# Performance work log

Hardware: AMD Instinct MI355X
Metric: run time of the kernel (lower is better)

Reference implementation:

```python
import jax, jax.numpy as jnp
import numpy as np

B, N, K = 8, 2048, 16
C_IN, C_MID, C_OUT = 64, 16, 64
WH = [32, 32]
FH = [256]


def _mlp_params(key, dims, scale_keyed=True):
    ps = []
    for i in range(len(dims) - 1):
        key, k1 = jax.random.split(key)
        w = jax.random.normal(k1, (dims[i], dims[i + 1]), jnp.float32) / np.sqrt(dims[i])
        b = jnp.zeros((dims[i + 1],), jnp.float32)
        ps += [w, b]
    return ps


def setup_inputs() -> dict:
    key = jax.random.key(0)
    k1, k2, k3, k4, k5 = jax.random.split(key, 5)
    groups = jnp.broadcast_to(jnp.arange(N, dtype=jnp.int32) // K, (B, N))
    points = jax.random.normal(k1, (B, N, 3), jnp.float32)
    feats = jax.random.normal(k2, (B, N, C_IN), jnp.float32)
    point_mask = (jax.random.uniform(k3, (B, N)) > 0.1).astype(jnp.float32)
    w1, b1, w2, b2, w3, b3 = _mlp_params(k4, [3] + WH + [C_MID])
    f1, fb1, f2, fb2 = _mlp_params(k5, [C_IN * C_MID] + FH + [C_OUT])
    return {"groups": groups, "points": points, "feats": feats,
            "point_mask": point_mask,
            "w1": w1, "b1": b1, "w2": w2, "b2": b2, "w3": w3, "b3": b3,
            "f1": f1, "fb1": fb1, "f2": f2, "fb2": fb2}


def _neighbor_idxs(groups):
    # matches[b,i,j] = groups[b,i]==groups[b,j]; torch .nonzero yields, per (b,i),
    # the matching j in increasing order -> stable argsort of ~matches, take first K.
    matches = groups[:, :, None] == groups[:, None, :]            # [B,N,N]
    return jnp.argsort((~matches).astype(jnp.int32), axis=-1)[:, :, :K]  # [B,N,K]


def reference(groups, points, feats, point_mask,
              w1, b1, w2, b2, w3, b3, f1, fb1, f2, fb2):
    idxs = _neighbor_idxs(groups)                                  # [B,N,K] int
    gather = jax.vmap(lambda arr, ix: arr[ix])                     # per-batch gather
    nb_pts = gather(points, idxs)                                  # [B,N,K,3]
    nb_feats = gather(feats, idxs)                                 # [B,N,K,C_IN]
    rel = points[:, :, None, :] - nb_pts                           # [B,N,K,3] (xy encoding = identity)

    # weight_conv: pointwise MLP 3 -> 32 -> 32 -> C_MID, then explicit ReLU
    h = jax.nn.relu(rel @ w1 + b1)
    h = jax.nn.relu(h @ w2 + b2)
    m = jax.nn.relu(h @ w3 + b3)                                   # [B,N,K,C_MID]

    tmask = gather(point_mask, idxs)                               # [B,N,K]
    m = m * tmask[..., None]
    nb_feats = nb_feats * tmask[..., None]

    # per-(point) matmul: [C_MID,K] x [K,C_IN] -> flatten C_MID-major
    e = jnp.einsum('bnkm,bnkc->bnmc', m, nb_feats)                 # [B,N,C_MID,C_IN]
    e = e.reshape(B, N, C_MID * C_IN)

    # final_conv: pointwise MLP 1024 -> 256 -> C_OUT
    h2 = jax.nn.relu(e @ f1 + fb1)
    out = h2 @ f2 + fb2                                            # [B,N,C_OUT]
    return out
```

## Files before the change

kernel.cpp:

```cpp
#include <hip/hip_runtime.h>

typedef unsigned short u16;
typedef short bf16x8 __attribute__((ext_vector_type(8)));
typedef float f32x4  __attribute__((ext_vector_type(4)));
typedef u16   u16x4  __attribute__((ext_vector_type(4)));

__device__ __forceinline__ u16 f2bf(float f) {
  union { float f; unsigned int i; } v; v.f = f;
  unsigned int r = (v.i + 0x7FFFu + ((v.i >> 16) & 1u)) >> 16;
  return (u16)r;
}

__global__ __launch_bounds__(256) void repack_k(const float* __restrict__ f1,
                                                const float* __restrict__ f2,
                                                u16* __restrict__ f1p,
                                                u16* __restrict__ f2p) {
  const int o = blockIdx.x * 256 + threadIdx.x;
  if (o < 262144) {
    const int j = o & 7, n = (o >> 3) & 255, kb = o >> 11;
    f1p[o] = f2bf(f1[(kb * 8 + j) * 256 + n]);
  }
  if (o < 16384) {
    const int j = o & 7, n = (o >> 3) & 63, kb = o >> 9;
    f2p[o] = f2bf(f2[(kb * 8 + j) * 64 + n]);
  }
}

__global__ __launch_bounds__(256) void mlp_einsum_k(
    const float* __restrict__ points, const float* __restrict__ feats,
    const float* __restrict__ pmask,
    const float* __restrict__ w1, const float* __restrict__ b1,
    const float* __restrict__ w2, const float* __restrict__ b2,
    const float* __restrict__ w3, const float* __restrict__ b3,
    const float* __restrict__ f1, const float* __restrict__ f2,
    u16* __restrict__ f1p, u16* __restrict__ f2p,
    u16* __restrict__ Eg) {
  const int gi = blockIdx.x;
  const int bb = blockIdx.y;
  const int base = gi * 16;
  const int t = threadIdx.x;

  __shared__ float Wl[1712];
  __shared__ float Pl[16][3];
  __shared__ float Mask[16];
  __shared__ float F[1024];
  __shared__ float Ml[16 * 16 * 17];

  {
    const int o = (bb * 128 + gi) * 256 + t;
    { const int j = o & 7, n = (o >> 3) & 255, kb = o >> 11;
      f1p[o] = f2bf(f1[(kb * 8 + j) * 256 + n]); }
    if (o < 16384) {
      const int j = o & 7, n = (o >> 3) & 63, kb = o >> 9;
      f2p[o] = f2bf(f2[(kb * 8 + j) * 64 + n]);
    }
  }

  for (int idx = t; idx < 96;   idx += 256) Wl[idx]        = w1[idx];
  for (int idx = t; idx < 32;   idx += 256) Wl[96 + idx]   = b1[idx];
  for (int idx = t; idx < 1024; idx += 256) Wl[128 + idx]  = w2[idx];
  for (int idx = t; idx < 32;   idx += 256) Wl[1152 + idx] = b2[idx];
  for (int idx = t; idx < 512;  idx += 256) Wl[1184 + idx] = w3[idx];
  for (int idx = t; idx < 16;   idx += 256) Wl[1696 + idx] = b3[idx];
  if (t < 16) {
    Mask[t] = pmask[bb * 2048 + base + t];
    const int p = (bb * 2048 + base + t) * 3;
    Pl[t][0] = points[p + 0];
    Pl[t][1] = points[p + 1];
    Pl[t][2] = points[p + 2];
  }
  __syncthreads();

  for (int e = t; e < 1024; e += 256) {
    const int k = e >> 6;
    F[e] = feats[(bb * 2048 + base) * 64 + e] * Mask[k];
  }
  {
    const int i = t >> 4, k = t & 15;
    const float r0 = Pl[i][0] - Pl[k][0];
    const float r1 = Pl[i][1] - Pl[k][1];
    const float r2 = Pl[i][2] - Pl[k][2];
    float h1[32];
#pragma unroll
    for (int o = 0; o < 32; ++o) {
      float a = Wl[96 + o];
      a = fmaf(r0, Wl[o], a);
      a = fmaf(r1, Wl[32 + o], a);
      a = fmaf(r2, Wl[64 + o], a);
      h1[o] = fmaxf(a, 0.f);
    }
    float h2[32];
#pragma unroll
    for (int o = 0; o < 32; ++o) h2[o] = Wl[1152 + o];
#pragma unroll
    for (int j = 0; j < 32; ++j) {
      const float hj = h1[j];
      const float* w = &Wl[128 + j * 32];
#pragma unroll
      for (int o = 0; o < 32; ++o) h2[o] = fmaf(hj, w[o], h2[o]);
    }
#pragma unroll
    for (int o = 0; o < 32; ++o) h2[o] = fmaxf(h2[o], 0.f);
    float mo[16];
#pragma unroll
    for (int o = 0; o < 16; ++o) mo[o] = Wl[1696 + o];
#pragma unroll
    for (int j = 0; j < 32; ++j) {
      const float hj = h2[j];
      const float* w = &Wl[1184 + j * 16];
#pragma unroll
      for (int o = 0; o < 16; ++o) mo[o] = fmaf(hj, w[o], mo[o]);
    }
    const float mk = Mask[k];
    float* Mrow = &Ml[(i * 16 + k) * 17];
#pragma unroll
    for (int o = 0; o < 16; ++o) Mrow[o] = fmaxf(mo[o], 0.f) * mk;
  }
  __syncthreads();

  {
    const int i = t >> 4;
    const int c0 = (t & 15) * 4;
    float acc[16][4] = {};
#pragma unroll
    for (int k = 0; k < 16; ++k) {
      const float* Fr = &F[k * 64 + c0];
      const float f0 = Fr[0], fA = Fr[1], fB = Fr[2], fC = Fr[3];
      const float* Mrow = &Ml[(i * 16 + k) * 17];
#pragma unroll
      for (int mi = 0; mi < 16; ++mi) {
        const float mv = Mrow[mi];
        acc[mi][0] = fmaf(mv, f0, acc[mi][0]);
        acc[mi][1] = fmaf(mv, fA, acc[mi][1]);
        acc[mi][2] = fmaf(mv, fB, acc[mi][2]);
        acc[mi][3] = fmaf(mv, fC, acc[mi][3]);
      }
    }
    u16* Erow = Eg + (size_t)(bb * 2048 + base + i) * 1024;
#pragma unroll
    for (int mi = 0; mi < 16; ++mi) {
      u16x4 v = { f2bf(acc[mi][0]), f2bf(acc[mi][1]),
                  f2bf(acc[mi][2]), f2bf(acc[mi][3]) };
      *(u16x4*)&Erow[mi * 64 + c0] = v;
    }
  }
}

#define STAGE(bf_, kc_)                                                        \
  do {                                                                         \
    const int rl_ = lane >> 3;                                       \
    const int sg_ = (lane & 7) ^ rl_;         \
    const u16* s0_ =                                                           \
        Eg + (size_t)(R + wv * 8 + rl_) * 1024 + (kc_) + sg_ * 8;              \
    u16* d0_ = &Asw[bf_][(wv * 8) * 64];            \
    u16* d1_ = &Asw[bf_][(32 + wv * 8) * 64];                                  \
    __builtin_amdgcn_global_load_lds(                                          \
        (const __attribute__((address_space(1))) void*)s0_,                    \
        (__attribute__((address_space(3))) void*)d0_, 16, 0, 0);               \
    __builtin_amdgcn_global_load_lds(                                          \
        (const __attribute__((address_space(1))) void*)(s0_ + 32 * 1024),      \
        (__attribute__((address_space(3))) void*)d1_, 16, 0, 0);               \
  } while (0)

__global__ __launch_bounds__(256) void gemm_k(
    const u16* __restrict__ Eg, const u16* __restrict__ f1p,
    const float* __restrict__ fb1, const u16* __restrict__ f2p,
    const float* __restrict__ fb2, float* __restrict__ out) {
  const int R = blockIdx.x * 64;
  const int t = threadIdx.x;
  const int wv = t >> 6, lane = t & 63;
  const int q = lane >> 4, r16 = lane & 15;

  __shared__ __align__(16) u16 Asw[2][64 * 64];
  __shared__ __align__(16) u16 H2[64 * 264];

  const int nb = wv * 64;
  f32x4 acc[4][4] = {};

  STAGE(0, 0);
  for (int c = 0; c < 16; ++c) {
    const int bf = c & 1;
    asm volatile("s_waitcnt vmcnt(0)" ::: "memory");
    __builtin_amdgcn_s_barrier();

    bf16x8 bv[2][4];
#pragma unroll
    for (int ksl = 0; ksl < 2; ++ksl) {
      const int kb = c * 8 + ksl * 4 + q;
#pragma unroll
      for (int nt = 0; nt < 4; ++nt)
        bv[ksl][nt] =
            *(const bf16x8*)&f1p[(size_t)(kb * 256 + nb + nt * 16 + r16) * 8];
    }
    bf16x8 a[2][4];
#pragma unroll
    for (int ksl = 0; ksl < 2; ++ksl)
#pragma unroll
      for (int rt = 0; rt < 4; ++rt) {
        const int r = rt * 16 + r16;
        const int g = (ksl * 4 + q) ^ (r & 7);
        a[ksl][rt] = *(const bf16x8*)&Asw[bf][r * 64 + g * 8];
      }
    __builtin_amdgcn_sched_barrier(0);
    if (c < 15) STAGE(bf ^ 1, (c + 1) * 64);
    __builtin_amdgcn_sched_barrier(0);
#pragma unroll
    for (int ksl = 0; ksl < 2; ++ksl)
#pragma unroll
      for (int nt = 0; nt < 4; ++nt)
#pragma unroll
        for (int rt = 0; rt < 4; ++rt)
          acc[rt][nt] = __builtin_amdgcn_mfma_f32_16x16x32_bf16(
              a[ksl][rt], bv[ksl][nt], acc[rt][nt], 0, 0, 0);
    __builtin_amdgcn_s_barrier();
  }

#pragma unroll
  for (int nt = 0; nt < 4; ++nt) {
    const int col = nb + nt * 16 + r16;
    const float bias = fb1[col];
#pragma unroll
    for (int rt = 0; rt < 4; ++rt)
#pragma unroll
      for (int r = 0; r < 4; ++r)
        H2[(rt * 16 + q * 4 + r) * 264 + col] =
            f2bf(fmaxf(acc[rt][nt][r] + bias, 0.f));
  }
  __syncthreads();

  const int n0 = wv * 16;
  const float bias2 = fb2[n0 + r16];
#pragma unroll
  for (int rt = 0; rt < 4; ++rt) {
    f32x4 a2 = {};
#pragma unroll
    for (int ks = 0; ks < 8; ++ks) {
      const bf16x8 av = *(const bf16x8*)&H2[(rt * 16 + r16) * 264 + ks * 32 + q * 8];
      const bf16x8 b2v =
          *(const bf16x8*)&f2p[(size_t)((ks * 4 + q) * 64 + n0 + r16) * 8];
      a2 = __builtin_amdgcn_mfma_f32_16x16x32_bf16(av, b2v, a2, 0, 0, 0);
    }
#pragma unroll
    for (int r = 0; r < 4; ++r)
      out[(size_t)(R + rt * 16 + q * 4 + r) * 64 + n0 + r16] = a2[r] + bias2;
  }
}
#undef STAGE

__global__ __launch_bounds__(256) void fused_k(
    const float* __restrict__ points, const float* __restrict__ feats,
    const float* __restrict__ pmask,
    const float* __restrict__ w1, const float* __restrict__ b1,
    const float* __restrict__ w2, const float* __restrict__ b2,
    const float* __restrict__ w3, const float* __restrict__ b3,
    const u16* __restrict__ f1p, const float* __restrict__ fb1,
    const u16* __restrict__ f2p, const float* __restrict__ fb2,
    float* __restrict__ out) {
  const int gi = blockIdx.x;
  const int bb = blockIdx.y;
  const int base = gi * 16;
  const int t = threadIdx.x;

  __shared__ float Wl[1712];
  __shared__ float Pl[16][3];
  __shared__ float Mask[16];
  __shared__ float F[1024];
  __shared__ __align__(16) u16 E[16 * 1032];
  __shared__ __align__(16) union {
    float Ml[16 * 16 * 17];
    u16   H2[16 * 264];
  } U;

  for (int idx = t; idx < 96;   idx += 256) Wl[idx]        = w1[idx];
  for (int idx = t; idx < 32;   idx += 256) Wl[96 + idx]   = b1[idx];
  for (int idx = t; idx < 1024; idx += 256) Wl[128 + idx]  = w2[idx];
  for (int idx = t; idx < 32;   idx += 256) Wl[1152 + idx] = b2[idx];
  for (int idx = t; idx < 512;  idx += 256) Wl[1184 + idx] = w3[idx];
  for (int idx = t; idx < 16;   idx += 256) Wl[1696 + idx] = b3[idx];
  if (t < 16) {
    Mask[t] = pmask[bb * 2048 + base + t];
    const int p = (bb * 2048 + base + t) * 3;
    Pl[t][0] = points[p + 0];
    Pl[t][1] = points[p + 1];
    Pl[t][2] = points[p + 2];
  }
  __syncthreads();

  for (int e = t; e < 1024; e += 256) {
    const int k = e >> 6;
    F[e] = feats[(bb * 2048 + base) * 64 + e] * Mask[k];
  }
  {
    const int i = t >> 4, k = t & 15;
    const float r0 = Pl[i][0] - Pl[k][0];
    const float r1 = Pl[i][1] - Pl[k][1];
    const float r2 = Pl[i][2] - Pl[k][2];
    float h1[32];
#pragma unroll
    for (int o = 0; o < 32; ++o) {
      float a = Wl[96 + o];
      a = fmaf(r0, Wl[o], a);
      a = fmaf(r1, Wl[32 + o], a);
      a = fmaf(r2, Wl[64 + o], a);
      h1[o] = fmaxf(a, 0.f);
    }
    float h2[32];
#pragma unroll
    for (int o = 0; o < 32; ++o) h2[o] = Wl[1152 + o];
#pragma unroll
    for (int j = 0; j < 32; ++j) {
      const float hj = h1[j];
      const float* w = &Wl[128 + j * 32];
#pragma unroll
      for (int o = 0; o < 32; ++o) h2[o] = fmaf(hj, w[o], h2[o]);
    }
#pragma unroll
    for (int o = 0; o < 32; ++o) h2[o] = fmaxf(h2[o], 0.f);
    float mo[16];
#pragma unroll
    for (int o = 0; o < 16; ++o) mo[o] = Wl[1696 + o];
#pragma unroll
    for (int j = 0; j < 32; ++j) {
      const float hj = h2[j];
      const float* w = &Wl[1184 + j * 16];
#pragma unroll
      for (int o = 0; o < 16; ++o) mo[o] = fmaf(hj, w[o], mo[o]);
    }
    const float mk = Mask[k];
    float* Mrow = &U.Ml[(i * 16 + k) * 17];
#pragma unroll
    for (int o = 0; o < 16; ++o) Mrow[o] = fmaxf(mo[o], 0.f) * mk;
  }
  __syncthreads();

  {
    const int i = t >> 4;
    const int c0 = (t & 15) * 4;
    float acc[16][4] = {};
#pragma unroll
    for (int k = 0; k < 16; ++k) {
      const float* Fr = &F[k * 64 + c0];
      const float f0 = Fr[0], fA = Fr[1], fB = Fr[2], fC = Fr[3];
      const float* Mrow = &U.Ml[(i * 16 + k) * 17];
#pragma unroll
      for (int mi = 0; mi < 16; ++mi) {
        const float mv = Mrow[mi];
        acc[mi][0] = fmaf(mv, f0, acc[mi][0]);
        acc[mi][1] = fmaf(mv, fA, acc[mi][1]);
        acc[mi][2] = fmaf(mv, fB, acc[mi][2]);
        acc[mi][3] = fmaf(mv, fC, acc[mi][3]);
      }
    }
    __syncthreads();
#pragma unroll
    for (int mi = 0; mi < 16; ++mi) {
      u16x4 v = { f2bf(acc[mi][0]), f2bf(acc[mi][1]), f2bf(acc[mi][2]), f2bf(acc[mi][3]) };
      *(u16x4*)&E[i * 1032 + mi * 64 + c0] = v;
    }
  }
  __syncthreads();

  {
    const int wv = t >> 6;
    const int lane = t & 63;
    const int q = lane >> 4, r16 = lane & 15;
    const int nb = wv * 64;
    f32x4 acc[4] = {};
    for (int ks = 0; ks < 32; ++ks) {
      const int k0 = ks * 32;
      const bf16x8 a = *(const bf16x8*)&E[r16 * 1032 + k0 + q * 8];
      const int kb = (k0 >> 3) + q;
#pragma unroll
      for (int nt = 0; nt < 4; ++nt) {
        const bf16x8 bvv = *(const bf16x8*)&f1p[(kb * 256 + nb + nt * 16 + r16) * 8];
        acc[nt] = __builtin_amdgcn_mfma_f32_16x16x32_bf16(a, bvv, acc[nt], 0, 0, 0);
      }
    }
    __syncthreads();
#pragma unroll
    for (int nt = 0; nt < 4; ++nt) {
      const int col = nb + nt * 16 + r16;
      const float bias = fb1[col];
#pragma unroll
      for (int r = 0; r < 4; ++r)
        U.H2[(q * 4 + r) * 264 + col] = f2bf(fmaxf(acc[nt][r] + bias, 0.f));
    }
  }
  __syncthreads();

  {
    const int wv = t >> 6;
    const int lane = t & 63;
    const int q = lane >> 4, r16 = lane & 15;
    const int n0 = wv * 16;
    f32x4 acc = {};
#pragma unroll
    for (int ks = 0; ks < 8; ++ks) {
      const int k0 = ks * 32;
      const bf16x8 a = *(const bf16x8*)&U.H2[r16 * 264 + k0 + q * 8];
      const bf16x8 bvv = *(const bf16x8*)&f2p[(((k0 >> 3) + q) * 64 + n0 + r16) * 8];
      acc = __builtin_amdgcn_mfma_f32_16x16x32_bf16(a, bvv, acc, 0, 0, 0);
    }
    const int col = n0 + r16;
    const float bias = fb2[col];
#pragma unroll
    for (int r = 0; r < 4; ++r) {
      const int row = q * 4 + r;
      out[((size_t)(bb * 2048 + base + row)) * 64 + col] = acc[r] + bias;
    }
  }
}

extern "C" void kernel_launch(void* const* d_in, const int* in_sizes, int n_in,
                              void* d_out, int out_size, void* d_ws, size_t ws_size,
                              hipStream_t stream) {
  const float* points = (const float*)d_in[1];
  const float* feats  = (const float*)d_in[2];
  const float* pmask  = (const float*)d_in[3];
  const float* w1 = (const float*)d_in[4];
  const float* b1 = (const float*)d_in[5];
  const float* w2 = (const float*)d_in[6];
  const float* b2 = (const float*)d_in[7];
  const float* w3 = (const float*)d_in[8];
  const float* b3 = (const float*)d_in[9];
  const float* f1 = (const float*)d_in[10];
  const float* fb1 = (const float*)d_in[11];
  const float* f2 = (const float*)d_in[12];
  const float* fb2 = (const float*)d_in[13];
  float* out = (float*)d_out;

  u16* f1p = (u16*)d_ws;
  u16* f2p = f1p + 262144;
  const size_t NEED = 524288 + 32768 + (size_t)16384 * 1024 * 2;

  if (ws_size >= NEED) {
    u16* Eg = f2p + 16384;
    mlp_einsum_k<<<dim3(128, 8), dim3(256), 0, stream>>>(
        points, feats, pmask, w1, b1, w2, b2, w3, b3, f1, f2, f1p, f2p, Eg);
    gemm_k<<<dim3(256), dim3(256), 0, stream>>>(Eg, f1p, fb1, f2p, fb2, out);
  } else {
    repack_k<<<dim3(1024), dim3(256), 0, stream>>>(f1, f2, f1p, f2p);
    fused_k<<<dim3(128, 8), dim3(256), 0, stream>>>(points, feats, pmask,
                                                    w1, b1, w2, b2, w3, b3,
                                                    f1p, fb1, f2p, fb2, out);
  }
}
```

Measured before the change: 140.0 us.

## Triple-buffer GEMM A staging and read MLP weights directly from global

The GEMM kernel moves from a double to a triple LDS buffer for A tiles. It prefetches two stages ahead with a partial vmcnt wait and drops the trailing barrier, so more load latency is hidden. The MLP/einsum kernel drops the LDS copy of the small weight-conv MLP weights and reads them straight from global memory, where they are uniform and cacheable. It also vectorizes the feature load, pads the M rows to stride 20, and adds an occupancy hint. Removing the trailing barrier leaves only the top-of-loop barrier to protect the buffer being overwritten, which relies on the three-buffer rotation being correct.

```diff
diff --git a/kernel.cpp b/kernel.cpp
--- a/kernel.cpp
+++ b/kernel.cpp
@@ -26,7 +26,7 @@
   }
 }
 
-__global__ __launch_bounds__(256) void mlp_einsum_k(
+__global__ __launch_bounds__(256, 4) void mlp_einsum_k(
     const float* __restrict__ points, const float* __restrict__ feats,
     const float* __restrict__ pmask,
     const float* __restrict__ w1, const float* __restrict__ b1,
@@ -40,11 +40,10 @@
   const int base = gi * 16;
   const int t = threadIdx.x;
 
-  __shared__ float Wl[1712];
   __shared__ float Pl[16][3];
   __shared__ float Mask[16];
   __shared__ float F[1024];
-  __shared__ float Ml[16 * 16 * 17];
+  __shared__ float Ml[16 * 16 * 20];
 
   {
     const int o = (bb * 128 + gi) * 256 + t;
@@ -56,12 +55,6 @@
     }
   }
 
-  for (int idx = t; idx < 96;   idx += 256) Wl[idx]        = w1[idx];
-  for (int idx = t; idx < 32;   idx += 256) Wl[96 + idx]   = b1[idx];
-  for (int idx = t; idx < 1024; idx += 256) Wl[128 + idx]  = w2[idx];
-  for (int idx = t; idx < 32;   idx += 256) Wl[1152 + idx] = b2[idx];
-  for (int idx = t; idx < 512;  idx += 256) Wl[1184 + idx] = w3[idx];
-  for (int idx = t; idx < 16;   idx += 256) Wl[1696 + idx] = b3[idx];
   if (t < 16) {
     Mask[t] = pmask[bb * 2048 + base + t];
     const int p = (bb * 2048 + base + t) * 3;
@@ -71,9 +64,13 @@
   }
   __syncthreads();
 
-  for (int e = t; e < 1024; e += 256) {
-    const int k = e >> 6;
-    F[e] = feats[(bb * 2048 + base) * 64 + e] * Mask[k];
+  {
+    const int k = t >> 4;
+    const float mk = Mask[k];
+    const f32x4 fv =
+        *(const f32x4*)&feats[(size_t)(bb * 2048 + base) * 64 + t * 4];
+    f32x4 fs = { fv.x * mk, fv.y * mk, fv.z * mk, fv.w * mk };
+    *(f32x4*)&F[t * 4] = fs;
   }
   {
     const int i = t >> 4, k = t & 15;
@@ -83,19 +80,19 @@
     float h1[32];
 #pragma unroll
     for (int o = 0; o < 32; ++o) {
-      float a = Wl[96 + o];
-      a = fmaf(r0, Wl[o], a);
-      a = fmaf(r1, Wl[32 + o], a);
-      a = fmaf(r2, Wl[64 + o], a);
+      float a = b1[o];
+      a = fmaf(r0, w1[o], a);
+      a = fmaf(r1, w1[32 + o], a);
+      a = fmaf(r2, w1[64 + o], a);
       h1[o] = fmaxf(a, 0.f);
     }
     float h2[32];
 #pragma unroll
-    for (int o = 0; o < 32; ++o) h2[o] = Wl[1152 + o];
+    for (int o = 0; o < 32; ++o) h2[o] = b2[o];
 #pragma unroll
     for (int j = 0; j < 32; ++j) {
       const float hj = h1[j];
-      const float* w = &Wl[128 + j * 32];
+      const float* w = &w2[j * 32];
 #pragma unroll
       for (int o = 0; o < 32; ++o) h2[o] = fmaf(hj, w[o], h2[o]);
     }
@@ -103,16 +100,16 @@
     for (int o = 0; o < 32; ++o) h2[o] = fmaxf(h2[o], 0.f);
     float mo[16];
 #pragma unroll
-    for (int o = 0; o < 16; ++o) mo[o] = Wl[1696 + o];
+    for (int o = 0; o < 16; ++o) mo[o] = b3[o];
 #pragma unroll
     for (int j = 0; j < 32; ++j) {
       const float hj = h2[j];
-      const float* w = &Wl[1184 + j * 16];
+      const float* w = &w3[j * 16];
 #pragma unroll
       for (int o = 0; o < 16; ++o) mo[o] = fmaf(hj, w[o], mo[o]);
     }
     const float mk = Mask[k];
-    float* Mrow = &Ml[(i * 16 + k) * 17];
+    float* Mrow = &Ml[(i * 16 + k) * 20];
 #pragma unroll
     for (int o = 0; o < 16; ++o) Mrow[o] = fmaxf(mo[o], 0.f) * mk;
   }
@@ -126,7 +123,7 @@
     for (int k = 0; k < 16; ++k) {
       const float* Fr = &F[k * 64 + c0];
       const float f0 = Fr[0], fA = Fr[1], fB = Fr[2], fC = Fr[3];
-      const float* Mrow = &Ml[(i * 16 + k) * 17];
+      const float* Mrow = &Ml[(i * 16 + k) * 20];
 #pragma unroll
       for (int mi = 0; mi < 16; ++mi) {
         const float mv = Mrow[mi];
@@ -171,16 +168,18 @@
   const int wv = t >> 6, lane = t & 63;
   const int q = lane >> 4, r16 = lane & 15;
 
-  __shared__ __align__(16) u16 Asw[2][64 * 64];
+  __shared__ __align__(16) u16 Asw[3][64 * 64];
   __shared__ __align__(16) u16 H2[64 * 264];
 
   const int nb = wv * 64;
   f32x4 acc[4][4] = {};
 
   STAGE(0, 0);
+  STAGE(1, 64);
+  int cur = 0, stg = 2;
   for (int c = 0; c < 16; ++c) {
-    const int bf = c & 1;
-    asm volatile("s_waitcnt vmcnt(0)" ::: "memory");
+    if (c < 15) asm volatile("s_waitcnt vmcnt(2)" ::: "memory");
+    else        asm volatile("s_waitcnt vmcnt(0)" ::: "memory");
     __builtin_amdgcn_s_barrier();
 
     bf16x8 bv[2][4];
@@ -199,10 +198,10 @@
       for (int rt = 0; rt < 4; ++rt) {
         const int r = rt * 16 + r16;
         const int g = (ksl * 4 + q) ^ (r & 7);
-        a[ksl][rt] = *(const bf16x8*)&Asw[bf][r * 64 + g * 8];
+        a[ksl][rt] = *(const bf16x8*)&Asw[cur][r * 64 + g * 8];
       }
     __builtin_amdgcn_sched_barrier(0);
-    if (c < 15) STAGE(bf ^ 1, (c + 1) * 64);
+    if (c <= 13) STAGE(stg, (c + 2) * 64);
     __builtin_amdgcn_sched_barrier(0);
 #pragma unroll
     for (int ksl = 0; ksl < 2; ++ksl)
@@ -212,7 +211,8 @@
         for (int rt = 0; rt < 4; ++rt)
           acc[rt][nt] = __builtin_amdgcn_mfma_f32_16x16x32_bf16(
               a[ksl][rt], bv[ksl][nt], acc[rt][nt], 0, 0, 0);
-    __builtin_amdgcn_s_barrier();
+    cur = (cur == 2) ? 0 : cur + 1;
+    stg = (stg == 2) ? 0 : stg + 1;
   }
 
 #pragma unroll
@@ -235,7 +235,8 @@
     f32x4 a2 = {};
 #pragma unroll
     for (int ks = 0; ks < 8; ++ks) {
-      const bf16x8 av = *(const bf16x8*)&H2[(rt * 16 + r16) * 264 + ks * 32 + q * 8];
+      const bf16x8 av =
+          *(const bf16x8*)&H2[(rt * 16 + r16) * 264 + ks * 32 + q * 8];
       const bf16x8 b2v =
           *(const bf16x8*)&f2p[(size_t)((ks * 4 + q) * 64 + n0 + r16) * 8];
       a2 = __builtin_amdgcn_mfma_f32_16x16x32_bf16(av, b2v, a2, 0, 0, 0);
```

New measurement: 130.0 us. 7.2% less time.
